# Performance work log

Hardware: AMD Instinct MI355X
Metric: run time of the kernel (lower is better)

## Reference

```python
import jax, jax.numpy as jnp
import numpy as np

B, T, H, HORIZON = 512, 256, 512, 64


def setup_inputs() -> dict:
    key = jax.random.key(0)
    ks = jax.random.split(key, 16)
    s = 1.0 / np.sqrt(H)  # PyTorch LSTM init bound

    def u(k, shape):
        return jax.random.uniform(k, shape, jnp.float32, -s, s)

    return {
        "x": jax.random.normal(ks[0], (B, T, 1), jnp.float32),
        "enc_Wih0": u(ks[1], (4 * H, 1)),
        "enc_Whh0": u(ks[2], (4 * H, H)),
        "enc_b0": u(ks[3], (4 * H,)),
        "enc_Wih1": u(ks[4], (4 * H, H)),
        "enc_Whh1": u(ks[5], (4 * H, H)),
        "enc_b1": u(ks[6], (4 * H,)),
        "dec_Wih0": u(ks[7], (4 * H, 1)),
        "dec_Whh0": u(ks[8], (4 * H, H)),
        "dec_b0": u(ks[9], (4 * H,)),
        "dec_Wih1": u(ks[10], (4 * H, H)),
        "dec_Whh1": u(ks[11], (4 * H, H)),
        "dec_b1": u(ks[12], (4 * H,)),
        "head_W": u(ks[13], (1, H)),
        "head_b": u(ks[14], (1,)),
    }


def _lstm_cell(x_t, h, c, Wih, Whh, b):
    # PyTorch gate order: input, forget, cell(g), output
    gates = x_t @ Wih.T + h @ Whh.T + b  # [B, 4H]
    i, f, g, o = jnp.split(gates, 4, axis=-1)
    i = jax.nn.sigmoid(i)
    f = jax.nn.sigmoid(f)
    g = jnp.tanh(g)
    o = jax.nn.sigmoid(o)
    c_new = f * c + i * g
    return o * jnp.tanh(c_new), c_new


def reference(x, enc_Wih0, enc_Whh0, enc_b0, enc_Wih1, enc_Whh1, enc_b1,
              dec_Wih0, dec_Whh0, dec_b0, dec_Wih1, dec_Whh1, dec_b1,
              head_W, head_b):
    b_sz = x.shape[0]
    hid = enc_Whh0.shape[1]
    z = jnp.zeros((b_sz, hid), x.dtype)

    # ---- encoder: 2-layer LSTM over time, keep only final (h, c) ----
    def enc_step(carry, x_t):
        h0, c0, h1, c1 = carry
        h0, c0 = _lstm_cell(x_t, h0, c0, enc_Wih0, enc_Whh0, enc_b0)
        h1, c1 = _lstm_cell(h0, h1, c1, enc_Wih1, enc_Whh1, enc_b1)
        return (h0, c0, h1, c1), None

    (h0, c0, h1, c1), _ = jax.lax.scan(enc_step, (z, z, z, z),
                                       jnp.swapaxes(x, 0, 1))  # time-major [T,B,1]

    dec_in = x[:, -1, :]  # [B, 1] last observed value

    def dec_step(carry, _):
        h0, c0, h1, c1, inp = carry
        h0, c0 = _lstm_cell(inp, h0, c0, dec_Wih0, dec_Whh0, dec_b0)
        h1, c1 = _lstm_cell(h0, h1, c1, dec_Wih1, dec_Whh1, dec_b1)
        step = h1 @ head_W.T + head_b  # [B, 1]
        return (h0, c0, h1, c1, step), step

    _, steps = jax.lax.scan(dec_step, (h0, c0, h1, c1, dec_in),
                            None, length=HORIZON)  # [HORIZON, B, 1]
    return jnp.swapaxes(steps[..., 0], 0, 1)  # [B, HORIZON]
```

## Files before the change

### kernel.cpp

```cpp
#include <hip/hip_runtime.h>
#include <math.h>

using ushort_t = unsigned short;
using short8 = __attribute__((ext_vector_type(8))) short;
using floatx16 = __attribute__((ext_vector_type(16))) float;
using int4v = __attribute__((ext_vector_type(4))) int;
using int2v = __attribute__((ext_vector_type(2))) int;

constexpr int kB = 512, kT = 256, kH = 512, kHor = 64;
constexpr int NG = 4 * kH;

__device__ __forceinline__ ushort_t f2bf(float v) {
  unsigned u = __builtin_bit_cast(unsigned, v);
  return (ushort_t)((u + 0x7FFFu + ((u >> 16) & 1u)) >> 16);
}
__device__ __forceinline__ float bf2f(ushort_t b) {
  unsigned u = (unsigned)b << 16;
  return __builtin_bit_cast(float, u);
}
__device__ __forceinline__ float sig_(float x) { return 1.0f / (1.0f + __expf(-x)); }

__device__ __forceinline__ void async16(const ushort_t* g, ushort_t* l) {
  __builtin_amdgcn_global_load_lds(
      (const __attribute__((address_space(1))) void*)g,
      (__attribute__((address_space(3))) void*)l, 16, 0, 0);
}

struct UnitP {
  const ushort_t *Whi, *Wlo;
  const ushort_t *B0hi, *B0lo;
  const ushort_t *B1hi, *B1lo;
  const float* bias;
  ushort_t *Hhi, *Hlo;
  int Kw;
};

struct EX {
  const float* xsrc; const float* wx; int xmode; int tcol;
  float* outp; int ocol;
  float* inp_next; const float* headb; int do_init;
  const float* headW; float* head_acc; int do_head;
};

struct Ptrs {
  const float* x;
  const ushort_t *w0eh, *w0el, *w1eh, *w1el;
  const ushort_t *w0dh, *w0dl, *w1dh, *w1dl;
  ushort_t *h0h[2], *h0l[2], *h1h[2], *h1l[2];
  const float *be0, *be1, *bd0, *bd1, *wxe, *wxd;
  float *ib0, *ib1;
  const float *hW, *hb;
  float* out;
  unsigned *bar1, *barR, *barG;
};

__device__ __forceinline__ void run_unit(const UnitP& U, const EX& E, const bool isB,
                                         const int mb, const int nb,
                                         ushort_t* sm, ushort_t* hshi, ushort_t* hslo,
                                         float* creg) {
  const int tid = threadIdx.x;
  const int m0blk = mb * 64;
  const int n0blk = nb * 64;
  const int nkt = U.Kw >> 6;

  const int wv = tid >> 6;
  const int ln = tid & 63;
  const int l31 = ln & 31;
  const int half = ln >> 5;
  const int wm = wv & 1, wn = wv >> 1;
  const int m0w = wm * 32, n0w = wn * 32;

  const int r8 = ln >> 3;
  const int k8s = (ln & 7) ^ r8;
  const bool stA = wv < 2;
  const ushort_t* gsrcA = (wv == 0) ? U.Whi : U.Wlo;
  const ushort_t* b0p = (wv == 2) ? U.B0hi : U.B0lo;
  const ushort_t* b1p = (wv == 2) ? U.B1hi : U.B1lo;
  ushort_t* lwb = &sm[wv * 4096];

  int4v breg[8];

  auto issueW = [&](int kt, int bufsel) {
    ushort_t* lb = lwb + bufsel * 16384;
    const ushort_t* g0 = gsrcA + (size_t)(m0blk + r8) * U.Kw + kt * 64 + k8s * 8;
    #pragma unroll
    for (int i = 0; i < 8; ++i)
      async16(g0 + (size_t)i * 8 * U.Kw, lb + i * 512);
  };
  auto issueB = [&](int kt) {
    const ushort_t* bsrc = (kt < 8) ? b0p : b1p;
    const int col0 = (kt & 7) * 64;
    const ushort_t* g0 = bsrc + (size_t)(n0blk + r8) * kH + col0 + k8s * 8;
    #pragma unroll
    for (int i = 0; i < 8; ++i)
      asm volatile("global_load_dwordx4 %0, %1, off sc0 sc1"
                   : "=v"(breg[i])
                   : "v"(g0 + (size_t)i * 8 * kH)
                   : "memory");
  };
  auto writeB = [&](int bufsel) {
    ushort_t* lb = lwb + bufsel * 16384;
    asm volatile("s_waitcnt vmcnt(0)" ::: "memory");
    #pragma unroll
    for (int i = 0; i < 8; ++i)
      *(int4v*)(lb + i * 512 + ln * 8) = breg[i];
    asm volatile("s_waitcnt lgkmcnt(0)" ::: "memory");
  };

  floatx16 acc;
  #pragma unroll
  for (int i = 0; i < 16; ++i) acc[i] = 0.0f;

  if (stA) issueW(0, 0); else issueB(0);

  for (int kt = 0; kt < nkt; ++kt) {
    const int cur = kt & 1;
    if (kt + 1 < nkt) {
      if (kt > 0) {
        asm volatile("" ::: "memory");
        __builtin_amdgcn_s_barrier();
        asm volatile("" ::: "memory");
      }
      if (stA) {
        issueW(kt + 1, cur ^ 1);
        asm volatile("" ::: "memory");
        __builtin_amdgcn_s_waitcnt(0xF78);
      } else {
        writeB(cur);
        issueB(kt + 1);
      }
    } else {
      if (stA) {
        asm volatile("" ::: "memory");
        __builtin_amdgcn_s_waitcnt(0xF70);
      } else {
        writeB(cur);
      }
    }
    asm volatile("" ::: "memory");
    __builtin_amdgcn_s_barrier();
    asm volatile("" ::: "memory");

    const ushort_t* base = &sm[cur * 16384];
    #pragma unroll
    for (int ks = 0; ks < 4; ++ks) {
      const int k8 = ks * 2 + half;
      const int qa = (m0w + l31) * 8 + (k8 ^ (l31 & 7));
      const int qb = (n0w + l31) * 8 + (k8 ^ (l31 & 7));
      short8 ahi = *(const short8*)(base + qa * 8);
      short8 alo = *(const short8*)(base + 4096 + qa * 8);
      short8 bhi = *(const short8*)(base + 8192 + qb * 8);
      short8 blo = *(const short8*)(base + 12288 + qb * 8);
      acc = __builtin_amdgcn_mfma_f32_32x32x16_bf16(alo, bhi, acc, 0, 0, 0);
      acc = __builtin_amdgcn_mfma_f32_32x32x16_bf16(ahi, blo, acc, 0, 0, 0);
      acc = __builtin_amdgcn_mfma_f32_32x32x16_bf16(ahi, bhi, acc, 0, 0, 0);
    }
  }

  const int jt0 = mb * 16;
  const int ng = n0blk + n0w + l31;
  float xv = 0.0f;
  if (!isB) {
    if (E.xmode == 0) xv = E.xsrc[(size_t)ng * kT + E.tcol];
    else xv = __hip_atomic_load((float*)&E.xsrc[ng], __ATOMIC_RELAXED,
                                __HIP_MEMORY_SCOPE_AGENT);
  }

  #pragma unroll
  for (int rg = 0; rg < 4; ++rg) {
    const int jl = wm * 8 + rg * 2 + half;
    const int jg = jt0 + jl;
    const float4 bi = *(const float4*)&U.bias[jg * 4];
    float gi = acc[rg * 4 + 0] + bi.x;
    float gf = acc[rg * 4 + 1] + bi.y;
    float gg = acc[rg * 4 + 2] + bi.z;
    float go = acc[rg * 4 + 3] + bi.w;
    if (!isB) {
      const float4 wx4 = *(const float4*)&E.wx[jg * 4];
      gi += xv * wx4.x; gf += xv * wx4.y; gg += xv * wx4.z; go += xv * wx4.w;
    }
    const float i_ = sig_(gi), f_ = sig_(gf), g_ = tanhf(gg), o_ = sig_(go);
    const float cn = f_ * creg[rg] + i_ * g_;
    creg[rg] = cn;
    const float hn = o_ * tanhf(cn);
    const ushort_t hhi = f2bf(hn);
    const ushort_t hlo = f2bf(hn - bf2f(hhi));
    const int nbk = n0w + l31;
    hshi[nbk * 18 + jl] = hhi;
    hslo[nbk * 18 + jl] = hlo;
  }
  __syncthreads();

  {
    const int nbk = tid >> 2;
    const int jq = (tid & 3) * 4;
    const unsigned a0 = hshi[nbk * 18 + jq + 0], a1 = hshi[nbk * 18 + jq + 1];
    const unsigned a2 = hshi[nbk * 18 + jq + 2], a3 = hshi[nbk * 18 + jq + 3];
    const unsigned b0 = hslo[nbk * 18 + jq + 0], b1 = hslo[nbk * 18 + jq + 1];
    const unsigned b2 = hslo[nbk * 18 + jq + 2], b3 = hslo[nbk * 18 + jq + 3];
    int2v vh, vl;
    vh[0] = (int)(a0 | (a1 << 16)); vh[1] = (int)(a2 | (a3 << 16));
    vl[0] = (int)(b0 | (b1 << 16)); vl[1] = (int)(b2 | (b3 << 16));
    ushort_t* ph = &U.Hhi[(size_t)(n0blk + nbk) * kH + jt0 + jq];
    ushort_t* pl = &U.Hlo[(size_t)(n0blk + nbk) * kH + jt0 + jq];
    asm volatile("global_store_dwordx2 %0, %1, off sc0 sc1"
                 :: "v"(ph), "v"(vh) : "memory");
    asm volatile("global_store_dwordx2 %0, %1, off sc0 sc1"
                 :: "v"(pl), "v"(vl) : "memory");
  }

  if (isB) {
    if (E.do_head && tid < 64) {
      float s = 0.0f;
      #pragma unroll
      for (int jb = 0; jb < 16; ++jb)
        s += (bf2f(hshi[tid * 18 + jb]) + bf2f(hslo[tid * 18 + jb])) * E.headW[jt0 + jb];
      atomicAdd(&E.head_acc[n0blk + tid], s);
    }
  } else if (mb == 0 && tid < 64) {
    const int n = n0blk + tid;
    if (E.do_init)
      __hip_atomic_store(&E.inp_next[n], E.headb[0], __ATOMIC_RELAXED,
                         __HIP_MEMORY_SCOPE_AGENT);
    if (E.ocol >= 0) {
      const float v = __hip_atomic_load((float*)&E.xsrc[n], __ATOMIC_RELAXED,
                                        __HIP_MEMORY_SCOPE_AGENT);
      E.outp[(size_t)n * kHor + E.ocol] = v;
    }
  }
}

__global__ __launch_bounds__(256, 2) void lstm_persist(Ptrs P) {
  __shared__ __align__(16) ushort_t sm[32768];
  __shared__ ushort_t hshi[64 * 18];
  __shared__ ushort_t hslo[64 * 18];

  const int tid = threadIdx.x;
  const int bx = blockIdx.x;
  const bool isB = bx >= 256;
  const int bid = isB ? bx - 256 : bx;
  const int xs = bid & 7;
  const int q = bid >> 3;
  const int mb = (q >> 3) * 8 + xs;
  const int nb = q & 7;

  float creg[4] = {0.0f, 0.0f, 0.0f, 0.0f};

  int gen = 0;
  auto gbar = [&]() {
    asm volatile("s_waitcnt vmcnt(0)" ::: "memory");
    __syncthreads();
    if (tid == 0) {
      unsigned old = __hip_atomic_fetch_add(&P.bar1[(bx & 63) * 32], 1u,
                         __ATOMIC_RELAXED, __HIP_MEMORY_SCOPE_AGENT);
      if (old == (unsigned)(gen * 8 + 7)) {
        unsigned o2 = __hip_atomic_fetch_add(P.barR, 1u,
                          __ATOMIC_RELAXED, __HIP_MEMORY_SCOPE_AGENT);
        if (o2 == (unsigned)(gen * 64 + 63))
          __hip_atomic_store(P.barG, (unsigned)(gen + 1),
                             __ATOMIC_RELAXED, __HIP_MEMORY_SCOPE_AGENT);
      }
      while (__hip_atomic_load(P.barG, __ATOMIC_RELAXED,
                               __HIP_MEMORY_SCOPE_AGENT) <= (unsigned)gen)
        __builtin_amdgcn_s_sleep(2);
    }
    __syncthreads();
    ++gen;
  };

  for (int p = 0; p <= kT; ++p) {
    const int rd = p & 1, wr = (p + 1) & 1;
    const bool active = isB ? (p >= 1) : (p < kT);
    if (active) {
      UnitP U; EX E = {};
      if (!isB) {
        U = UnitP{P.w0eh, P.w0el, P.h0h[rd], P.h0l[rd], P.h0h[rd], P.h0l[rd],
                  P.be0, P.h0h[wr], P.h0l[wr], 512};
        E.xsrc = P.x; E.wx = P.wxe; E.xmode = 0; E.tcol = p; E.ocol = -1;
      } else {
        U = UnitP{P.w1eh, P.w1el, P.h0h[rd], P.h0l[rd], P.h1h[rd], P.h1l[rd],
                  P.be1, P.h1h[wr], P.h1l[wr], 1024};
        E.ocol = -1;
      }
      run_unit(U, E, isB, mb, nb, sm, hshi, hslo, creg);
    }
    gbar();
  }

  for (int t = 0; t < kHor; ++t) {
    const int r0 = t & 1, w0i = (t + 1) & 1;
    const int r1 = (t + 1) & 1, w1i = t & 1;
    float* ibr = (t & 1) ? P.ib1 : P.ib0;
    float* ibw = (t & 1) ? P.ib0 : P.ib1;
    if (!isB) {
      UnitP U = {P.w0dh, P.w0dl, P.h0h[r0], P.h0l[r0], P.h0h[r0], P.h0l[r0],
                 P.bd0, P.h0h[w0i], P.h0l[w0i], 512};
      EX E = {};
      E.wx = P.wxd;
      if (t == 0) { E.xsrc = P.x; E.xmode = 0; E.tcol = 255; E.ocol = -1; }
      else        { E.xsrc = ibr; E.xmode = 1; E.ocol = t - 1; E.outp = P.out; }
      E.do_init = 1; E.inp_next = ibw; E.headb = P.hb;
      run_unit(U, E, false, mb, nb, sm, hshi, hslo, creg);
    }
    gbar();
    if (isB) {
      UnitP U = {P.w1dh, P.w1dl, P.h0h[w0i], P.h0l[w0i], P.h1h[r1], P.h1l[r1],
                 P.bd1, P.h1h[w1i], P.h1l[w1i], 1024};
      EX E = {};
      E.ocol = -1;
      E.do_head = 1; E.headW = P.hW; E.head_acc = ibw;
      run_unit(U, E, true, mb, nb, sm, hshi, hslo, creg);
    }
    gbar();
  }

  if (!isB && mb == 0 && tid < 64) {
    const int n = nb * 64 + tid;
    P.out[(size_t)n * kHor + 63] =
        __hip_atomic_load(P.ib0 + n, __ATOMIC_RELAXED, __HIP_MEMORY_SCOPE_AGENT);
  }
}

__global__ void prep_w(const float* __restrict__ s0, const float* __restrict__ s1,
                       ushort_t* __restrict__ hi, ushort_t* __restrict__ lo, int Kw) {
  const int k = blockIdx.x * 256 + threadIdx.x;
  const int r = blockIdx.y;
  const int j = r >> 2, g = r & 3;
  const int srow = g * kH + j;
  const float v = (k < kH) ? s0[(size_t)srow * kH + k]
                           : s1[(size_t)srow * kH + (k - kH)];
  const ushort_t h = f2bf(v);
  const ushort_t l = f2bf(v - bf2f(h));
  hi[(size_t)r * Kw + k] = h;
  lo[(size_t)r * Kw + k] = l;
}

__global__ void prep_vec(const float* __restrict__ src, float* __restrict__ dst) {
  const int t = blockIdx.x * 256 + threadIdx.x;
  const int j = t >> 2, g = t & 3;
  dst[t] = src[g * kH + j];
}

__global__ void init_zero(ushort_t* p0, ushort_t* p1, ushort_t* p2, ushort_t* p3,
                          ushort_t* p4, ushort_t* p5, ushort_t* p6, ushort_t* p7) {
  const int i = blockIdx.x * 256 + threadIdx.x;
  p0[i] = 0; p1[i] = 0; p2[i] = 0; p3[i] = 0;
  p4[i] = 0; p5[i] = 0; p6[i] = 0; p7[i] = 0;
}

__global__ void init_bar(unsigned* b) {
  const int i = blockIdx.x * 256 + threadIdx.x;
  if (i < 2112) b[i] = 0;
}

extern "C" void kernel_launch(void* const* d_in, const int* in_sizes, int n_in,
                              void* d_out, int out_size, void* d_ws, size_t ws_size,
                              hipStream_t stream) {
  const float* x     = (const float*)d_in[0];
  const float* eWih0 = (const float*)d_in[1];
  const float* eWhh0 = (const float*)d_in[2];
  const float* eb0   = (const float*)d_in[3];
  const float* eWih1 = (const float*)d_in[4];
  const float* eWhh1 = (const float*)d_in[5];
  const float* eb1   = (const float*)d_in[6];
  const float* dWih0 = (const float*)d_in[7];
  const float* dWhh0 = (const float*)d_in[8];
  const float* db0   = (const float*)d_in[9];
  const float* dWih1 = (const float*)d_in[10];
  const float* dWhh1 = (const float*)d_in[11];
  const float* db1   = (const float*)d_in[12];
  const float* hW    = (const float*)d_in[13];
  const float* hb    = (const float*)d_in[14];
  float* out = (float*)d_out;

  char* w = (char*)d_ws;
  size_t off = 0;
  auto aus = [&](size_t n) { ushort_t* p = (ushort_t*)(w + off); off += ((n * 2 + 255) & ~(size_t)255); return p; };
  auto afl = [&](size_t n) { float* p = (float*)(w + off); off += ((n * 4 + 255) & ~(size_t)255); return p; };

  ushort_t* w0e_hi = aus((size_t)NG * 512); ushort_t* w0e_lo = aus((size_t)NG * 512);
  ushort_t* w1e_hi = aus((size_t)NG * 1024); ushort_t* w1e_lo = aus((size_t)NG * 1024);
  ushort_t* w0d_hi = aus((size_t)NG * 512); ushort_t* w0d_lo = aus((size_t)NG * 512);
  ushort_t* w1d_hi = aus((size_t)NG * 1024); ushort_t* w1d_lo = aus((size_t)NG * 1024);
  ushort_t* h0hi[2] = {aus(kB * kH), aus(kB * kH)};
  ushort_t* h0lo[2] = {aus(kB * kH), aus(kB * kH)};
  ushort_t* h1hi[2] = {aus(kB * kH), aus(kB * kH)};
  ushort_t* h1lo[2] = {aus(kB * kH), aus(kB * kH)};
  float* be0 = afl(NG); float* be1 = afl(NG);
  float* bd0 = afl(NG); float* bd1 = afl(NG);
  float* wxe = afl(NG); float* wxd = afl(NG);
  float* ib0 = afl(kB); float* ib1 = afl(kB);
  unsigned* barb = (unsigned*)(w + off); off += ((2112 * 4 + 255) & ~(size_t)255);

  prep_w<<<dim3(2, NG), 256, 0, stream>>>(eWhh0, eWhh0, w0e_hi, w0e_lo, 512);
  prep_w<<<dim3(4, NG), 256, 0, stream>>>(eWih1, eWhh1, w1e_hi, w1e_lo, 1024);
  prep_w<<<dim3(2, NG), 256, 0, stream>>>(dWhh0, dWhh0, w0d_hi, w0d_lo, 512);
  prep_w<<<dim3(4, NG), 256, 0, stream>>>(dWih1, dWhh1, w1d_hi, w1d_lo, 1024);
  prep_vec<<<8, 256, 0, stream>>>(eb0, be0);
  prep_vec<<<8, 256, 0, stream>>>(eb1, be1);
  prep_vec<<<8, 256, 0, stream>>>(db0, bd0);
  prep_vec<<<8, 256, 0, stream>>>(db1, bd1);
  prep_vec<<<8, 256, 0, stream>>>(eWih0, wxe);
  prep_vec<<<8, 256, 0, stream>>>(dWih0, wxd);
  init_zero<<<1024, 256, 0, stream>>>(h0hi[0], h0hi[1], h0lo[0], h0lo[1],
                                      h1hi[0], h1hi[1], h1lo[0], h1lo[1]);
  init_bar<<<9, 256, 0, stream>>>(barb);

  Ptrs P = {};
  P.x = x;
  P.w0eh = w0e_hi; P.w0el = w0e_lo; P.w1eh = w1e_hi; P.w1el = w1e_lo;
  P.w0dh = w0d_hi; P.w0dl = w0d_lo; P.w1dh = w1d_hi; P.w1dl = w1d_lo;
  P.h0h[0] = h0hi[0]; P.h0h[1] = h0hi[1];
  P.h0l[0] = h0lo[0]; P.h0l[1] = h0lo[1];
  P.h1h[0] = h1hi[0]; P.h1h[1] = h1hi[1];
  P.h1l[0] = h1lo[0]; P.h1l[1] = h1lo[1];
  P.be0 = be0; P.be1 = be1; P.bd0 = bd0; P.bd1 = bd1;
  P.wxe = wxe; P.wxd = wxd;
  P.ib0 = ib0; P.ib1 = ib1;
  P.hW = hW; P.hb = hb;
  P.out = out;
  P.bar1 = barb; P.barR = barb + 2048; P.barG = barb + 2080;

  lstm_persist<<<512, 256, 0, stream>>>(P);
}
```

Baseline: 6.142 ms.

## Double M-tile per block, stream weights from global, triple-buffer hidden state in LDS

Each block now covers 128 gate rows instead of 64, which halves the persistent grid from 512 to 256 blocks and changes the barrier fan-in from 8 to 4 arrivals per slot. Weight fragments are read straight from global memory into registers, so only the hidden-state (B) tiles are staged through LDS, using a three-buffer register-prefetch pipeline. Each wave now runs two 32x32 MFMA accumulators, and the h writeback uses wider 16-byte stores. The aim is fewer blocks to synchronise and less LDS traffic per step. The cost is higher register pressure (launch bounds drop to 1 block per CU) and weight loads that depend on cache hits rather than being coalesced through LDS.

Result: slower. 15.76 ms (+156.6%).

```diff
diff --git a/kernel.cpp b/kernel.cpp
--- a/kernel.cpp
+++ b/kernel.cpp
@@ -5,7 +5,6 @@
 using short8 = __attribute__((ext_vector_type(8))) short;
 using floatx16 = __attribute__((ext_vector_type(16))) float;
 using int4v = __attribute__((ext_vector_type(4))) int;
-using int2v = __attribute__((ext_vector_type(2))) int;
 
 constexpr int kB = 512, kT = 256, kH = 512, kHor = 64;
 constexpr int NG = 4 * kH;
@@ -19,12 +18,6 @@
   return __builtin_bit_cast(float, u);
 }
 __device__ __forceinline__ float sig_(float x) { return 1.0f / (1.0f + __expf(-x)); }
-
-__device__ __forceinline__ void async16(const ushort_t* g, ushort_t* l) {
-  __builtin_amdgcn_global_load_lds(
-      (const __attribute__((address_space(1))) void*)g,
-      (__attribute__((address_space(3))) void*)l, 16, 0, 0);
-}
 
 struct UnitP {
   const ushort_t *Whi, *Wlo;
@@ -59,7 +52,7 @@
                                          ushort_t* sm, ushort_t* hshi, ushort_t* hslo,
                                          float* creg) {
   const int tid = threadIdx.x;
-  const int m0blk = mb * 64;
+  const int m0blk = mb * 128;
   const int n0blk = nb * 64;
   const int nkt = U.Kw >> 6;
 
@@ -68,97 +61,101 @@
   const int l31 = ln & 31;
   const int half = ln >> 5;
   const int wm = wv & 1, wn = wv >> 1;
-  const int m0w = wm * 32, n0w = wn * 32;
-
-  const int r8 = ln >> 3;
-  const int k8s = (ln & 7) ^ r8;
-  const bool stA = wv < 2;
-  const ushort_t* gsrcA = (wv == 0) ? U.Whi : U.Wlo;
-  const ushort_t* b0p = (wv == 2) ? U.B0hi : U.B0lo;
-  const ushort_t* b1p = (wv == 2) ? U.B1hi : U.B1lo;
-  ushort_t* lwb = &sm[wv * 4096];
-
-  int4v breg[8];
-
-  auto issueW = [&](int kt, int bufsel) {
-    ushort_t* lb = lwb + bufsel * 16384;
-    const ushort_t* g0 = gsrcA + (size_t)(m0blk + r8) * U.Kw + kt * 64 + k8s * 8;
-    #pragma unroll
-    for (int i = 0; i < 8; ++i)
-      async16(g0 + (size_t)i * 8 * U.Kw, lb + i * 512);
+
+  const size_t rowA = (size_t)(m0blk + wm * 64 + l31) * U.Kw;
+  const ushort_t* aHi0 = U.Whi + rowA;
+  const ushort_t* aLo0 = U.Wlo + rowA;
+  const ushort_t* aHi1 = aHi0 + (size_t)32 * U.Kw;
+  const ushort_t* aLo1 = aLo0 + (size_t)32 * U.Kw;
+
+  const int sn0 = tid >> 3;
+  const int sk8 = (tid & 7) ^ (sn0 & 7);
+  const size_t g0off = (size_t)(n0blk + sn0) * kH + sk8 * 8;
+  const size_t g1off = g0off + (size_t)32 * kH;
+
+  auto issueB = [&](int ktc, int4v& r0, int4v& r1, int4v& r2, int4v& r3) {
+    const ushort_t* bhiP = (ktc < 8) ? U.B0hi : U.B1hi;
+    const ushort_t* bloP = (ktc < 8) ? U.B0lo : U.B1lo;
+    const int col0 = (ktc & 7) * 64;
+    const ushort_t* p0 = bhiP + g0off + col0;
+    const ushort_t* p1 = bhiP + g1off + col0;
+    const ushort_t* p2 = bloP + g0off + col0;
+    const ushort_t* p3 = bloP + g1off + col0;
+    asm volatile("global_load_dwordx4 %0, %1, off sc0 sc1" : "=v"(r0) : "v"(p0) : "memory");
+    asm volatile("global_load_dwordx4 %0, %1, off sc0 sc1" : "=v"(r1) : "v"(p1) : "memory");
+    asm volatile("global_load_dwordx4 %0, %1, off sc0 sc1" : "=v"(r2) : "v"(p2) : "memory");
+    asm volatile("global_load_dwordx4 %0, %1, off sc0 sc1" : "=v"(r3) : "v"(p3) : "memory");
   };
-  auto issueB = [&](int kt) {
-    const ushort_t* bsrc = (kt < 8) ? b0p : b1p;
-    const int col0 = (kt & 7) * 64;
-    const ushort_t* g0 = bsrc + (size_t)(n0blk + r8) * kH + col0 + k8s * 8;
-    #pragma unroll
-    for (int i = 0; i < 8; ++i)
-      asm volatile("global_load_dwordx4 %0, %1, off sc0 sc1"
-                   : "=v"(breg[i])
-                   : "v"(g0 + (size_t)i * 8 * kH)
-                   : "memory");
+  auto writeBuf = [&](int bufsel, int4v r0, int4v r1, int4v r2, int4v r3) {
+    ushort_t* b = sm + bufsel * 8192;
+    *(int4v*)(b + tid * 8) = r0;
+    *(int4v*)(b + 2048 + tid * 8) = r1;
+    *(int4v*)(b + 4096 + tid * 8) = r2;
+    *(int4v*)(b + 6144 + tid * 8) = r3;
   };
-  auto writeB = [&](int bufsel) {
-    ushort_t* lb = lwb + bufsel * 16384;
-    asm volatile("s_waitcnt vmcnt(0)" ::: "memory");
-    #pragma unroll
-    for (int i = 0; i < 8; ++i)
-      *(int4v*)(lb + i * 512 + ln * 8) = breg[i];
-    asm volatile("s_waitcnt lgkmcnt(0)" ::: "memory");
-  };
-
-  floatx16 acc;
+
+  floatx16 acc0, acc1;
   #pragma unroll
-  for (int i = 0; i < 16; ++i) acc[i] = 0.0f;
-
-  if (stA) issueW(0, 0); else issueB(0);
-
-  for (int kt = 0; kt < nkt; ++kt) {
-    const int cur = kt & 1;
-    if (kt + 1 < nkt) {
-      if (kt > 0) {
-        asm volatile("" ::: "memory");
-        __builtin_amdgcn_s_barrier();
-        asm volatile("" ::: "memory");
-      }
-      if (stA) {
-        issueW(kt + 1, cur ^ 1);
-        asm volatile("" ::: "memory");
-        __builtin_amdgcn_s_waitcnt(0xF78);
-      } else {
-        writeB(cur);
-        issueB(kt + 1);
-      }
-    } else {
-      if (stA) {
-        asm volatile("" ::: "memory");
-        __builtin_amdgcn_s_waitcnt(0xF70);
-      } else {
-        writeB(cur);
-      }
-    }
-    asm volatile("" ::: "memory");
-    __builtin_amdgcn_s_barrier();
-    asm volatile("" ::: "memory");
-
-    const ushort_t* base = &sm[cur * 16384];
+  for (int i = 0; i < 16; ++i) { acc0[i] = 0.0f; acc1[i] = 0.0f; }
+
+  auto compute = [&](int bufsel, int kt) {
+    const ushort_t* base = sm + bufsel * 8192;
     #pragma unroll
     for (int ks = 0; ks < 4; ++ks) {
       const int k8 = ks * 2 + half;
-      const int qa = (m0w + l31) * 8 + (k8 ^ (l31 & 7));
-      const int qb = (n0w + l31) * 8 + (k8 ^ (l31 & 7));
-      short8 ahi = *(const short8*)(base + qa * 8);
-      short8 alo = *(const short8*)(base + 4096 + qa * 8);
-      short8 bhi = *(const short8*)(base + 8192 + qb * 8);
-      short8 blo = *(const short8*)(base + 12288 + qb * 8);
-      acc = __builtin_amdgcn_mfma_f32_32x32x16_bf16(alo, bhi, acc, 0, 0, 0);
-      acc = __builtin_amdgcn_mfma_f32_32x32x16_bf16(ahi, blo, acc, 0, 0, 0);
-      acc = __builtin_amdgcn_mfma_f32_32x32x16_bf16(ahi, bhi, acc, 0, 0, 0);
-    }
-  }
-
-  const int jt0 = mb * 16;
-  const int ng = n0blk + n0w + l31;
+      const int qb = (wn * 32 + l31) * 8 + (k8 ^ (l31 & 7));
+      short8 bhi = *(const short8*)(base + qb * 8);
+      short8 blo = *(const short8*)(base + 4096 + qb * 8);
+      const int off = kt * 64 + k8 * 8;
+      short8 a0h = *(const short8*)(aHi0 + off);
+      short8 a0l = *(const short8*)(aLo0 + off);
+      short8 a1h = *(const short8*)(aHi1 + off);
+      short8 a1l = *(const short8*)(aLo1 + off);
+      acc0 = __builtin_amdgcn_mfma_f32_32x32x16_bf16(a0l, bhi, acc0, 0, 0, 0);
+      acc0 = __builtin_amdgcn_mfma_f32_32x32x16_bf16(a0h, blo, acc0, 0, 0, 0);
+      acc0 = __builtin_amdgcn_mfma_f32_32x32x16_bf16(a0h, bhi, acc0, 0, 0, 0);
+      acc1 = __builtin_amdgcn_mfma_f32_32x32x16_bf16(a1l, bhi, acc1, 0, 0, 0);
+      acc1 = __builtin_amdgcn_mfma_f32_32x32x16_bf16(a1h, blo, acc1, 0, 0, 0);
+      acc1 = __builtin_amdgcn_mfma_f32_32x32x16_bf16(a1h, bhi, acc1, 0, 0, 0);
+    }
+  };
+
+  int4v e0, e1, e2, e3, o0, o1, o2, o3;
+
+  issueB(0, e0, e1, e2, e3);
+  issueB(1, o0, o1, o2, o3);
+  asm volatile("s_waitcnt vmcnt(4)" ::: "memory");
+  writeBuf(0, e0, e1, e2, e3);
+  issueB(2, e0, e1, e2, e3);
+
+  for (int kt = 0; kt < nkt; kt += 2) {
+    {
+      if (kt + 2 < nkt) { asm volatile("s_waitcnt vmcnt(4)" ::: "memory"); }
+      else              { asm volatile("s_waitcnt vmcnt(0)" ::: "memory"); }
+      writeBuf((kt + 1) % 3, o0, o1, o2, o3);
+      asm volatile("s_waitcnt lgkmcnt(0)" ::: "memory");
+      __builtin_amdgcn_s_barrier();
+      asm volatile("" ::: "memory");
+      compute(kt % 3, kt);
+      if (kt + 3 < nkt) issueB(kt + 3, o0, o1, o2, o3);
+    }
+    {
+      const int k2 = kt + 1;
+      if (k2 + 2 < nkt) { asm volatile("s_waitcnt vmcnt(4)" ::: "memory"); }
+      else              { asm volatile("s_waitcnt vmcnt(0)" ::: "memory"); }
+      if (k2 + 1 < nkt) writeBuf((k2 + 1) % 3, e0, e1, e2, e3);
+      asm volatile("s_waitcnt lgkmcnt(0)" ::: "memory");
+      __builtin_amdgcn_s_barrier();
+      asm volatile("" ::: "memory");
+      compute(k2 % 3, k2);
+      if (k2 + 3 < nkt) issueB(k2 + 3, e0, e1, e2, e3);
+    }
+  }
+  asm volatile("s_waitcnt vmcnt(0)" ::: "memory");
+
+  const int jt0 = mb * 32;
+  const int nlane = wn * 32 + l31;
+  const int ng = n0blk + nlane;
   float xv = 0.0f;
   if (!isB) {
     if (E.xmode == 0) xv = E.xsrc[(size_t)ng * kT + E.tcol];
@@ -167,54 +164,50 @@
   }
 
   #pragma unroll
-  for (int rg = 0; rg < 4; ++rg) {
-    const int jl = wm * 8 + rg * 2 + half;
-    const int jg = jt0 + jl;
-    const float4 bi = *(const float4*)&U.bias[jg * 4];
-    float gi = acc[rg * 4 + 0] + bi.x;
-    float gf = acc[rg * 4 + 1] + bi.y;
-    float gg = acc[rg * 4 + 2] + bi.z;
-    float go = acc[rg * 4 + 3] + bi.w;
-    if (!isB) {
-      const float4 wx4 = *(const float4*)&E.wx[jg * 4];
-      gi += xv * wx4.x; gf += xv * wx4.y; gg += xv * wx4.z; go += xv * wx4.w;
-    }
-    const float i_ = sig_(gi), f_ = sig_(gf), g_ = tanhf(gg), o_ = sig_(go);
-    const float cn = f_ * creg[rg] + i_ * g_;
-    creg[rg] = cn;
-    const float hn = o_ * tanhf(cn);
-    const ushort_t hhi = f2bf(hn);
-    const ushort_t hlo = f2bf(hn - bf2f(hhi));
-    const int nbk = n0w + l31;
-    hshi[nbk * 18 + jl] = hhi;
-    hslo[nbk * 18 + jl] = hlo;
+  for (int mt = 0; mt < 2; ++mt) {
+    const floatx16& ac = mt ? acc1 : acc0;
+    #pragma unroll
+    for (int rg = 0; rg < 4; ++rg) {
+      const int jl = wm * 16 + mt * 8 + rg * 2 + half;
+      const int jg = jt0 + jl;
+      const float4 bi = *(const float4*)&U.bias[jg * 4];
+      float gi = ac[rg * 4 + 0] + bi.x;
+      float gf = ac[rg * 4 + 1] + bi.y;
+      float gg = ac[rg * 4 + 2] + bi.z;
+      float go = ac[rg * 4 + 3] + bi.w;
+      if (!isB) {
+        const float4 wx4 = *(const float4*)&E.wx[jg * 4];
+        gi += xv * wx4.x; gf += xv * wx4.y; gg += xv * wx4.z; go += xv * wx4.w;
+      }
+      const float i_ = sig_(gi), f_ = sig_(gf), g_ = tanhf(gg), o_ = sig_(go);
+      const float cn = f_ * creg[mt * 4 + rg] + i_ * g_;
+      creg[mt * 4 + rg] = cn;
+      const float hn = o_ * tanhf(cn);
+      const ushort_t hhi = f2bf(hn);
+      const ushort_t hlo = f2bf(hn - bf2f(hhi));
+      hshi[nlane * 48 + jl] = hhi;
+      hslo[nlane * 48 + jl] = hlo;
+    }
   }
   __syncthreads();
 
   {
-    const int nbk = tid >> 2;
-    const int jq = (tid & 3) * 4;
-    const unsigned a0 = hshi[nbk * 18 + jq + 0], a1 = hshi[nbk * 18 + jq + 1];
-    const unsigned a2 = hshi[nbk * 18 + jq + 2], a3 = hshi[nbk * 18 + jq + 3];
-    const unsigned b0 = hslo[nbk * 18 + jq + 0], b1 = hslo[nbk * 18 + jq + 1];
-    const unsigned b2 = hslo[nbk * 18 + jq + 2], b3 = hslo[nbk * 18 + jq + 3];
-    int2v vh, vl;
-    vh[0] = (int)(a0 | (a1 << 16)); vh[1] = (int)(a2 | (a3 << 16));
-    vl[0] = (int)(b0 | (b1 << 16)); vl[1] = (int)(b2 | (b3 << 16));
-    ushort_t* ph = &U.Hhi[(size_t)(n0blk + nbk) * kH + jt0 + jq];
-    ushort_t* pl = &U.Hlo[(size_t)(n0blk + nbk) * kH + jt0 + jq];
-    asm volatile("global_store_dwordx2 %0, %1, off sc0 sc1"
-                 :: "v"(ph), "v"(vh) : "memory");
-    asm volatile("global_store_dwordx2 %0, %1, off sc0 sc1"
-                 :: "v"(pl), "v"(vl) : "memory");
+    const int nl = tid >> 2;
+    const int jq = (tid & 3) * 8;
+    int4v vh = *(const int4v*)&hshi[nl * 48 + jq];
+    int4v vl = *(const int4v*)&hslo[nl * 48 + jq];
+    ushort_t* ph = &U.Hhi[(size_t)(n0blk + nl) * kH + jt0 + jq];
+    ushort_t* pl = &U.Hlo[(size_t)(n0blk + nl) * kH + jt0 + jq];
+    asm volatile("global_store_dwordx4 %0, %1, off sc0 sc1" :: "v"(ph), "v"(vh) : "memory");
+    asm volatile("global_store_dwordx4 %0, %1, off sc0 sc1" :: "v"(pl), "v"(vl) : "memory");
   }
 
   if (isB) {
     if (E.do_head && tid < 64) {
       float s = 0.0f;
       #pragma unroll
-      for (int jb = 0; jb < 16; ++jb)
-        s += (bf2f(hshi[tid * 18 + jb]) + bf2f(hslo[tid * 18 + jb])) * E.headW[jt0 + jb];
+      for (int jb = 0; jb < 32; ++jb)
+        s += (bf2f(hshi[tid * 48 + jb]) + bf2f(hslo[tid * 48 + jb])) * E.headW[jt0 + jb];
       atomicAdd(&E.head_acc[n0blk + tid], s);
     }
   } else if (mb == 0 && tid < 64) {
@@ -230,21 +223,21 @@
   }
 }
 
-__global__ __launch_bounds__(256, 2) void lstm_persist(Ptrs P) {
-  __shared__ __align__(16) ushort_t sm[32768];
-  __shared__ ushort_t hshi[64 * 18];
-  __shared__ ushort_t hslo[64 * 18];
+__global__ __launch_bounds__(256, 1) void lstm_persist(Ptrs P) {
+  __shared__ __align__(16) ushort_t sm[3 * 8192];
+  __shared__ __align__(16) ushort_t hshi[64 * 48];
+  __shared__ __align__(16) ushort_t hslo[64 * 48];
 
   const int tid = threadIdx.x;
   const int bx = blockIdx.x;
-  const bool isB = bx >= 256;
-  const int bid = isB ? bx - 256 : bx;
+  const bool isB = bx >= 128;
+  const int bid = isB ? bx - 128 : bx;
   const int xs = bid & 7;
   const int q = bid >> 3;
-  const int mb = (q >> 3) * 8 + xs;
+  const int mb = xs + 8 * (q >> 3);
   const int nb = q & 7;
 
-  float creg[4] = {0.0f, 0.0f, 0.0f, 0.0f};
+  float creg[8] = {0.f, 0.f, 0.f, 0.f, 0.f, 0.f, 0.f, 0.f};
 
   int gen = 0;
   auto gbar = [&]() {
@@ -253,7 +246,7 @@
     if (tid == 0) {
       unsigned old = __hip_atomic_fetch_add(&P.bar1[(bx & 63) * 32], 1u,
                          __ATOMIC_RELAXED, __HIP_MEMORY_SCOPE_AGENT);
-      if (old == (unsigned)(gen * 8 + 7)) {
+      if (old == (unsigned)(gen * 4 + 3)) {
         unsigned o2 = __hip_atomic_fetch_add(P.barR, 1u,
                           __ATOMIC_RELAXED, __HIP_MEMORY_SCOPE_AGENT);
         if (o2 == (unsigned)(gen * 64 + 63))
@@ -421,5 +414,5 @@
   P.out = out;
   P.bar1 = barb; P.barR = barb + 2048; P.barG = barb + 2080;
 
-  lstm_persist<<<512, 256, 0, stream>>>(P);
-}
+  lstm_persist<<<256, 256, 0, stream>>>(P);
+}
```

## Spread A/B tile loads across all waves with deeper register prefetch of B

Applied to the files above, without the earlier changes.

Before this, two waves loaded the weight tiles through async LDS loads and the other two waves loaded the hidden-state tiles through registers. Now all four waves share both loads. B tiles are prefetched two k-steps ahead in two register sets, and the loop is unrolled by two with explicit vmcnt waits. The aim is to balance load issue across waves and hide global latency of the coherent hidden-state reads behind MFMA work. In exchange it uses more registers and needs more careful waitcnt bookkeeping, where an error would corrupt results.

Result: slower. 7.050 ms (+14.8%).

```diff
diff --git a/kernel.cpp b/kernel.cpp
--- a/kernel.cpp
+++ b/kernel.cpp
@@ -72,90 +72,111 @@
 
   const int r8 = ln >> 3;
   const int k8s = (ln & 7) ^ r8;
-  const bool stA = wv < 2;
-  const ushort_t* gsrcA = (wv == 0) ? U.Whi : U.Wlo;
-  const ushort_t* b0p = (wv == 2) ? U.B0hi : U.B0lo;
-  const ushort_t* b1p = (wv == 2) ? U.B1hi : U.B1lo;
-  ushort_t* lwb = &sm[wv * 4096];
-
-  int4v breg[8];
-
-  auto issueW = [&](int kt, int bufsel) {
-    ushort_t* lb = lwb + bufsel * 16384;
-    const ushort_t* g0 = gsrcA + (size_t)(m0blk + r8) * U.Kw + kt * 64 + k8s * 8;
+  const ushort_t* gsrcA = (wv < 2) ? U.Whi : U.Wlo;
+  const size_t aRowOff = (size_t)(m0blk + (wv & 1) * 32 + r8) * U.Kw + k8s * 8;
+  const int aLds = ((wv < 2) ? 0 : 4096) + (wv & 1) * 2048;
+
+  auto issueA = [&](int kt, int bufsel) {
+    ushort_t* lb = sm + bufsel * 8192 + aLds;
+    const ushort_t* g0 = gsrcA + aRowOff + kt * 64;
     #pragma unroll
-    for (int i = 0; i < 8; ++i)
+    for (int i = 0; i < 4; ++i)
       async16(g0 + (size_t)i * 8 * U.Kw, lb + i * 512);
   };
-  auto issueB = [&](int kt) {
-    const ushort_t* bsrc = (kt < 8) ? b0p : b1p;
-    const int col0 = (kt & 7) * 64;
-    const ushort_t* g0 = bsrc + (size_t)(n0blk + r8) * kH + col0 + k8s * 8;
-    #pragma unroll
-    for (int i = 0; i < 8; ++i)
-      asm volatile("global_load_dwordx4 %0, %1, off sc0 sc1"
-                   : "=v"(breg[i])
-                   : "v"(g0 + (size_t)i * 8 * kH)
-                   : "memory");
+
+  const int brow = tid >> 3;
+  const int bk8 = (tid & 7) ^ (brow & 7);
+  const size_t bOff0 = (size_t)(n0blk + brow) * kH + bk8 * 8;
+  const size_t bOff1 = bOff0 + (size_t)32 * kH;
+
+  auto issueBset = [&](int ktc, int4v* s) {
+    const ushort_t* bhiP = (ktc < 8) ? U.B0hi : U.B1hi;
+    const ushort_t* bloP = (ktc < 8) ? U.B0lo : U.B1lo;
+    const int col0 = (ktc & 7) * 64;
+    asm volatile("global_load_dwordx4 %0, %1, off sc0 sc1"
+                 : "=v"(s[0]) : "v"(bhiP + bOff0 + col0) : "memory");
+    asm volatile("global_load_dwordx4 %0, %1, off sc0 sc1"
+                 : "=v"(s[1]) : "v"(bhiP + bOff1 + col0) : "memory");
+    asm volatile("global_load_dwordx4 %0, %1, off sc0 sc1"
+                 : "=v"(s[2]) : "v"(bloP + bOff0 + col0) : "memory");
+    asm volatile("global_load_dwordx4 %0, %1, off sc0 sc1"
+                 : "=v"(s[3]) : "v"(bloP + bOff1 + col0) : "memory");
   };
-  auto writeB = [&](int bufsel) {
-    ushort_t* lb = lwb + bufsel * 16384;
-    asm volatile("s_waitcnt vmcnt(0)" ::: "memory");
-    #pragma unroll
-    for (int i = 0; i < 8; ++i)
-      *(int4v*)(lb + i * 512 + ln * 8) = breg[i];
-    asm volatile("s_waitcnt lgkmcnt(0)" ::: "memory");
+  auto writeBset = [&](int bufsel, const int4v* s) {
+    ushort_t* b = sm + 16384 + bufsel * 8192;
+    *(int4v*)(b + tid * 8) = s[0];
+    *(int4v*)(b + 2048 + tid * 8) = s[1];
+    *(int4v*)(b + 4096 + tid * 8) = s[2];
+    *(int4v*)(b + 6144 + tid * 8) = s[3];
   };
 
   floatx16 acc;
   #pragma unroll
   for (int i = 0; i < 16; ++i) acc[i] = 0.0f;
 
-  if (stA) issueW(0, 0); else issueB(0);
-
-  for (int kt = 0; kt < nkt; ++kt) {
-    const int cur = kt & 1;
-    if (kt + 1 < nkt) {
+  auto compute = [&](int bufsel) {
+    const ushort_t* ba = sm + bufsel * 8192;
+    const ushort_t* bb = sm + 16384 + bufsel * 8192;
+    #pragma unroll
+    for (int ks = 0; ks < 4; ++ks) {
+      const int k8 = ks * 2 + half;
+      const int qa = (m0w + l31) * 8 + (k8 ^ (l31 & 7));
+      const int qb = (n0w + l31) * 8 + (k8 ^ (l31 & 7));
+      short8 ahi = *(const short8*)(ba + qa * 8);
+      short8 alo = *(const short8*)(ba + 4096 + qa * 8);
+      short8 bhi = *(const short8*)(bb + qb * 8);
+      short8 blo = *(const short8*)(bb + 4096 + qb * 8);
+      acc = __builtin_amdgcn_mfma_f32_32x32x16_bf16(alo, bhi, acc, 0, 0, 0);
+      acc = __builtin_amdgcn_mfma_f32_32x32x16_bf16(ahi, blo, acc, 0, 0, 0);
+      acc = __builtin_amdgcn_mfma_f32_32x32x16_bf16(ahi, bhi, acc, 0, 0, 0);
+    }
+  };
+
+  int4v s0[4], s1[4];
+
+  issueBset(0, s0);
+  issueBset(1, s1);
+  issueA(0, 0);
+  asm volatile("s_waitcnt vmcnt(8)" ::: "memory");
+  writeBset(0, s0);
+  asm volatile("s_waitcnt lgkmcnt(0)" ::: "memory");
+  issueBset(2, s0);
+
+  for (int kt = 0; kt < nkt; kt += 2) {
+    {
       if (kt > 0) {
         asm volatile("" ::: "memory");
         __builtin_amdgcn_s_barrier();
         asm volatile("" ::: "memory");
       }
-      if (stA) {
-        issueW(kt + 1, cur ^ 1);
-        asm volatile("" ::: "memory");
-        __builtin_amdgcn_s_waitcnt(0xF78);
-      } else {
-        writeB(cur);
-        issueB(kt + 1);
-      }
-    } else {
-      if (stA) {
-        asm volatile("" ::: "memory");
-        __builtin_amdgcn_s_waitcnt(0xF70);
-      } else {
-        writeB(cur);
-      }
-    }
-    asm volatile("" ::: "memory");
-    __builtin_amdgcn_s_barrier();
-    asm volatile("" ::: "memory");
-
-    const ushort_t* base = &sm[cur * 16384];
-    #pragma unroll
-    for (int ks = 0; ks < 4; ++ks) {
-      const int k8 = ks * 2 + half;
-      const int qa = (m0w + l31) * 8 + (k8 ^ (l31 & 7));
-      const int qb = (n0w + l31) * 8 + (k8 ^ (l31 & 7));
-      short8 ahi = *(const short8*)(base + qa * 8);
-      short8 alo = *(const short8*)(base + 4096 + qa * 8);
-      short8 bhi = *(const short8*)(base + 8192 + qb * 8);
-      short8 blo = *(const short8*)(base + 12288 + qb * 8);
-      acc = __builtin_amdgcn_mfma_f32_32x32x16_bf16(alo, bhi, acc, 0, 0, 0);
-      acc = __builtin_amdgcn_mfma_f32_32x32x16_bf16(ahi, blo, acc, 0, 0, 0);
-      acc = __builtin_amdgcn_mfma_f32_32x32x16_bf16(ahi, bhi, acc, 0, 0, 0);
-    }
-  }
+      if (kt + 2 < nkt) { asm volatile("s_waitcnt vmcnt(4)" ::: "memory"); }
+      else              { asm volatile("s_waitcnt vmcnt(0)" ::: "memory"); }
+      writeBset(1, s1);
+      asm volatile("s_waitcnt lgkmcnt(0)" ::: "memory");
+      issueA(kt + 1, 1);
+      if (kt + 3 < nkt) issueBset(kt + 3, s1);
+      asm volatile("" ::: "memory");
+      __builtin_amdgcn_s_barrier();
+      asm volatile("" ::: "memory");
+      compute(0);
+    }
+    {
+      asm volatile("" ::: "memory");
+      __builtin_amdgcn_s_barrier();
+      asm volatile("" ::: "memory");
+      if (kt + 3 < nkt) { asm volatile("s_waitcnt vmcnt(4)" ::: "memory"); }
+      else              { asm volatile("s_waitcnt vmcnt(0)" ::: "memory"); }
+      if (kt + 2 < nkt) writeBset(0, s0);
+      asm volatile("s_waitcnt lgkmcnt(0)" ::: "memory");
+      if (kt + 2 < nkt) issueA(kt + 2, 0);
+      if (kt + 4 < nkt) issueBset(kt + 4, s0);
+      asm volatile("" ::: "memory");
+      __builtin_amdgcn_s_barrier();
+      asm volatile("" ::: "memory");
+      compute(1);
+    }
+  }
+  asm volatile("s_waitcnt vmcnt(0)" ::: "memory");
 
   const int jt0 = mb * 16;
   const int ng = n0blk + n0w + l31;
@@ -232,8 +253,8 @@
 
 __global__ __launch_bounds__(256, 2) void lstm_persist(Ptrs P) {
   __shared__ __align__(16) ushort_t sm[32768];
-  __shared__ ushort_t hshi[64 * 18];
-  __shared__ ushort_t hslo[64 * 18];
+  __shared__ __align__(16) ushort_t hshi[64 * 18];
+  __shared__ __align__(16) ushort_t hslo[64 * 18];
 
   const int tid = threadIdx.x;
   const int bx = blockIdx.x;
```

## Retile LSTM gate GEMM to 128x32 blocks with all waves streaming weights

Applied to the files above, without the earlier changes.

Changes each block's tile from 64 gate rows × 64 batch columns to 128 gate rows × 32 batch columns. The 16×16 grid of blocks per layer becomes 16 row groups by 16 batch groups, and each wave now owns a 32-row slice against the full 32 batch columns. All four waves async-load weight (hi/lo) tiles, and the small hidden-state B tile is loaded cooperatively by all threads through registers. The aim is to spread weight streaming across every wave and shrink the per-block hidden-state traffic. The trade-off is more weight bytes per block per step, a larger LDS footprint (hidden-state staging now aliases the A buffer), and a different wait-count pipeline.

New measurement: 8.746 ms. 42.4% more time.

```diff
diff --git a/kernel.cpp b/kernel.cpp
--- a/kernel.cpp
+++ b/kernel.cpp
@@ -9,6 +9,7 @@
 
 constexpr int kB = 512, kT = 256, kH = 512, kHor = 64;
 constexpr int NG = 4 * kH;
+constexpr int HSP = 48;
 
 __device__ __forceinline__ ushort_t f2bf(float v) {
   unsigned u = __builtin_bit_cast(unsigned, v);
@@ -56,109 +57,103 @@
 
 __device__ __forceinline__ void run_unit(const UnitP& U, const EX& E, const bool isB,
                                          const int mb, const int nb,
-                                         ushort_t* sm, ushort_t* hshi, ushort_t* hslo,
-                                         float* creg) {
+                                         ushort_t* sm, float* creg) {
   const int tid = threadIdx.x;
-  const int m0blk = mb * 64;
-  const int n0blk = nb * 64;
+  const int m0blk = mb * 128;
+  const int n0blk = nb * 32;
   const int nkt = U.Kw >> 6;
 
   const int wv = tid >> 6;
   const int ln = tid & 63;
   const int l31 = ln & 31;
   const int half = ln >> 5;
-  const int wm = wv & 1, wn = wv >> 1;
-  const int m0w = wm * 32, n0w = wn * 32;
+  const int m0w = wv * 32;
 
   const int r8 = ln >> 3;
   const int k8s = (ln & 7) ^ r8;
-  const bool stA = wv < 2;
-  const ushort_t* gsrcA = (wv == 0) ? U.Whi : U.Wlo;
-  const ushort_t* b0p = (wv == 2) ? U.B0hi : U.B0lo;
-  const ushort_t* b1p = (wv == 2) ? U.B1hi : U.B1lo;
-  ushort_t* lwb = &sm[wv * 4096];
-
-  int4v breg[8];
-
-  auto issueW = [&](int kt, int bufsel) {
-    ushort_t* lb = lwb + bufsel * 16384;
-    const ushort_t* g0 = gsrcA + (size_t)(m0blk + r8) * U.Kw + kt * 64 + k8s * 8;
+  const ushort_t* gsrcA = (wv < 2) ? U.Whi : U.Wlo;
+  const size_t aRowOff = (size_t)(m0blk + (wv & 1) * 64 + r8) * U.Kw + k8s * 8;
+  const int aLds = ((wv < 2) ? 0 : 8192) + (wv & 1) * 4096;
+
+  auto issueA = [&](int kt, int bufsel) {
+    ushort_t* lb = sm + bufsel * 16384 + aLds;
+    const ushort_t* g0 = gsrcA + aRowOff + kt * 64;
     #pragma unroll
     for (int i = 0; i < 8; ++i)
       async16(g0 + (size_t)i * 8 * U.Kw, lb + i * 512);
   };
-  auto issueB = [&](int kt) {
-    const ushort_t* bsrc = (kt < 8) ? b0p : b1p;
-    const int col0 = (kt & 7) * 64;
-    const ushort_t* g0 = bsrc + (size_t)(n0blk + r8) * kH + col0 + k8s * 8;
-    #pragma unroll
-    for (int i = 0; i < 8; ++i)
-      asm volatile("global_load_dwordx4 %0, %1, off sc0 sc1"
-                   : "=v"(breg[i])
-                   : "v"(g0 + (size_t)i * 8 * kH)
-                   : "memory");
+
+  const int brow = tid >> 3;
+  const int bk8 = (tid & 7) ^ (brow & 7);
+  const size_t bOff = (size_t)(n0blk + brow) * kH + bk8 * 8;
+
+  int4v rh, rl;
+  auto issueB = [&](int ktc) {
+    const ushort_t* bh = (ktc < 8) ? U.B0hi : U.B1hi;
+    const ushort_t* bl = (ktc < 8) ? U.B0lo : U.B1lo;
+    const int col0 = (ktc & 7) * 64;
+    asm volatile("global_load_dwordx4 %0, %1, off sc0 sc1"
+                 : "=v"(rh) : "v"(bh + bOff + col0) : "memory");
+    asm volatile("global_load_dwordx4 %0, %1, off sc0 sc1"
+                 : "=v"(rl) : "v"(bl + bOff + col0) : "memory");
   };
   auto writeB = [&](int bufsel) {
-    ushort_t* lb = lwb + bufsel * 16384;
-    asm volatile("s_waitcnt vmcnt(0)" ::: "memory");
-    #pragma unroll
-    for (int i = 0; i < 8; ++i)
-      *(int4v*)(lb + i * 512 + ln * 8) = breg[i];
-    asm volatile("s_waitcnt lgkmcnt(0)" ::: "memory");
+    ushort_t* b = sm + 32768 + bufsel * 4096;
+    *(int4v*)(b + tid * 8) = rh;
+    *(int4v*)(b + 2048 + tid * 8) = rl;
   };
 
   floatx16 acc;
   #pragma unroll
   for (int i = 0; i < 16; ++i) acc[i] = 0.0f;
 
-  if (stA) issueW(0, 0); else issueB(0);
-
-  for (int kt = 0; kt < nkt; ++kt) {
-    const int cur = kt & 1;
-    if (kt + 1 < nkt) {
-      if (kt > 0) {
-        asm volatile("" ::: "memory");
-        __builtin_amdgcn_s_barrier();
-        asm volatile("" ::: "memory");
-      }
-      if (stA) {
-        issueW(kt + 1, cur ^ 1);
-        asm volatile("" ::: "memory");
-        __builtin_amdgcn_s_waitcnt(0xF78);
-      } else {
-        writeB(cur);
-        issueB(kt + 1);
-      }
-    } else {
-      if (stA) {
-        asm volatile("" ::: "memory");
-        __builtin_amdgcn_s_waitcnt(0xF70);
-      } else {
-        writeB(cur);
-      }
-    }
-    asm volatile("" ::: "memory");
-    __builtin_amdgcn_s_barrier();
-    asm volatile("" ::: "memory");
-
-    const ushort_t* base = &sm[cur * 16384];
+  auto compute = [&](int bufsel) {
+    const ushort_t* ba = sm + bufsel * 16384;
+    const ushort_t* bb = sm + 32768 + bufsel * 4096;
     #pragma unroll
     for (int ks = 0; ks < 4; ++ks) {
       const int k8 = ks * 2 + half;
       const int qa = (m0w + l31) * 8 + (k8 ^ (l31 & 7));
-      const int qb = (n0w + l31) * 8 + (k8 ^ (l31 & 7));
-      short8 ahi = *(const short8*)(base + qa * 8);
-      short8 alo = *(const short8*)(base + 4096 + qa * 8);
-      short8 bhi = *(const short8*)(base + 8192 + qb * 8);
-      short8 blo = *(const short8*)(base + 12288 + qb * 8);
+      const int qb = l31 * 8 + (k8 ^ (l31 & 7));
+      short8 ahi = *(const short8*)(ba + qa * 8);
+      short8 alo = *(const short8*)(ba + 8192 + qa * 8);
+      short8 bhi = *(const short8*)(bb + qb * 8);
+      short8 blo = *(const short8*)(bb + 2048 + qb * 8);
       acc = __builtin_amdgcn_mfma_f32_32x32x16_bf16(alo, bhi, acc, 0, 0, 0);
       acc = __builtin_amdgcn_mfma_f32_32x32x16_bf16(ahi, blo, acc, 0, 0, 0);
       acc = __builtin_amdgcn_mfma_f32_32x32x16_bf16(ahi, bhi, acc, 0, 0, 0);
     }
-  }
-
-  const int jt0 = mb * 16;
-  const int ng = n0blk + n0w + l31;
+  };
+
+  issueA(0, 0);
+  issueB(0);
+
+  for (int kt = 0; kt < nkt; ++kt) {
+    if (kt > 0) {
+      asm volatile("" ::: "memory");
+      __builtin_amdgcn_s_barrier();
+      asm volatile("" ::: "memory");
+    }
+    if (kt + 1 < nkt) {
+      issueA(kt + 1, (kt + 1) & 1);
+      asm volatile("s_waitcnt vmcnt(8)" ::: "memory");
+    } else {
+      asm volatile("s_waitcnt vmcnt(0)" ::: "memory");
+    }
+    writeB(kt & 1);
+    asm volatile("s_waitcnt lgkmcnt(0)" ::: "memory");
+    if (kt + 1 < nkt) issueB(kt + 1);
+    asm volatile("" ::: "memory");
+    __builtin_amdgcn_s_barrier();
+    asm volatile("" ::: "memory");
+    compute(kt & 1);
+  }
+  asm volatile("s_waitcnt vmcnt(0)" ::: "memory");
+
+  ushort_t* hshi = sm;
+  ushort_t* hslo = sm + 2048;
+  const int jt0 = mb * 32;
+  const int ng = n0blk + l31;
   float xv = 0.0f;
   if (!isB) {
     if (E.xmode == 0) xv = E.xsrc[(size_t)ng * kT + E.tcol];
@@ -168,7 +163,7 @@
 
   #pragma unroll
   for (int rg = 0; rg < 4; ++rg) {
-    const int jl = wm * 8 + rg * 2 + half;
+    const int jl = wv * 8 + rg * 2 + half;
     const int jg = jt0 + jl;
     const float4 bi = *(const float4*)&U.bias[jg * 4];
     float gi = acc[rg * 4 + 0] + bi.x;
@@ -185,24 +180,23 @@
     const float hn = o_ * tanhf(cn);
     const ushort_t hhi = f2bf(hn);
     const ushort_t hlo = f2bf(hn - bf2f(hhi));
-    const int nbk = n0w + l31;
-    hshi[nbk * 18 + jl] = hhi;
-    hslo[nbk * 18 + jl] = hlo;
+    hshi[l31 * HSP + jl] = hhi;
+    hslo[l31 * HSP + jl] = hlo;
   }
   __syncthreads();
 
   {
-    const int nbk = tid >> 2;
-    const int jq = (tid & 3) * 4;
-    const unsigned a0 = hshi[nbk * 18 + jq + 0], a1 = hshi[nbk * 18 + jq + 1];
-    const unsigned a2 = hshi[nbk * 18 + jq + 2], a3 = hshi[nbk * 18 + jq + 3];
-    const unsigned b0 = hslo[nbk * 18 + jq + 0], b1 = hslo[nbk * 18 + jq + 1];
-    const unsigned b2 = hslo[nbk * 18 + jq + 2], b3 = hslo[nbk * 18 + jq + 3];
+    const int nl = tid >> 3;
+    const int jq = (tid & 7) * 4;
+    const unsigned a0 = hshi[nl * HSP + jq + 0], a1 = hshi[nl * HSP + jq + 1];
+    const unsigned a2 = hshi[nl * HSP + jq + 2], a3 = hshi[nl * HSP + jq + 3];
+    const unsigned b0 = hslo[nl * HSP + jq + 0], b1 = hslo[nl * HSP + jq + 1];
+    const unsigned b2 = hslo[nl * HSP + jq + 2], b3 = hslo[nl * HSP + jq + 3];
     int2v vh, vl;
     vh[0] = (int)(a0 | (a1 << 16)); vh[1] = (int)(a2 | (a3 << 16));
     vl[0] = (int)(b0 | (b1 << 16)); vl[1] = (int)(b2 | (b3 << 16));
-    ushort_t* ph = &U.Hhi[(size_t)(n0blk + nbk) * kH + jt0 + jq];
-    ushort_t* pl = &U.Hlo[(size_t)(n0blk + nbk) * kH + jt0 + jq];
+    ushort_t* ph = &U.Hhi[(size_t)(n0blk + nl) * kH + jt0 + jq];
+    ushort_t* pl = &U.Hlo[(size_t)(n0blk + nl) * kH + jt0 + jq];
     asm volatile("global_store_dwordx2 %0, %1, off sc0 sc1"
                  :: "v"(ph), "v"(vh) : "memory");
     asm volatile("global_store_dwordx2 %0, %1, off sc0 sc1"
@@ -210,14 +204,14 @@
   }
 
   if (isB) {
-    if (E.do_head && tid < 64) {
+    if (E.do_head && tid < 32) {
       float s = 0.0f;
       #pragma unroll
-      for (int jb = 0; jb < 16; ++jb)
-        s += (bf2f(hshi[tid * 18 + jb]) + bf2f(hslo[tid * 18 + jb])) * E.headW[jt0 + jb];
+      for (int jb = 0; jb < 32; ++jb)
+        s += (bf2f(hshi[tid * HSP + jb]) + bf2f(hslo[tid * HSP + jb])) * E.headW[jt0 + jb];
       atomicAdd(&E.head_acc[n0blk + tid], s);
     }
-  } else if (mb == 0 && tid < 64) {
+  } else if (mb == 0 && tid < 32) {
     const int n = n0blk + tid;
     if (E.do_init)
       __hip_atomic_store(&E.inp_next[n], E.headb[0], __ATOMIC_RELAXED,
@@ -231,9 +225,7 @@
 }
 
 __global__ __launch_bounds__(256, 2) void lstm_persist(Ptrs P) {
-  __shared__ __align__(16) ushort_t sm[32768];
-  __shared__ ushort_t hshi[64 * 18];
-  __shared__ ushort_t hslo[64 * 18];
+  __shared__ __align__(16) ushort_t sm[40960];
 
   const int tid = threadIdx.x;
   const int bx = blockIdx.x;
@@ -241,8 +233,8 @@
   const int bid = isB ? bx - 256 : bx;
   const int xs = bid & 7;
   const int q = bid >> 3;
-  const int mb = (q >> 3) * 8 + xs;
-  const int nb = q & 7;
+  const int mb = xs + 8 * (q >> 4);
+  const int nb = q & 15;
 
   float creg[4] = {0.0f, 0.0f, 0.0f, 0.0f};
 
@@ -282,7 +274,7 @@
                   P.be1, P.h1h[wr], P.h1l[wr], 1024};
         E.ocol = -1;
       }
-      run_unit(U, E, isB, mb, nb, sm, hshi, hslo, creg);
+      run_unit(U, E, isB, mb, nb, sm, creg);
     }
     gbar();
   }
@@ -300,7 +292,7 @@
       if (t == 0) { E.xsrc = P.x; E.xmode = 0; E.tcol = 255; E.ocol = -1; }
       else        { E.xsrc = ibr; E.xmode = 1; E.ocol = t - 1; E.outp = P.out; }
       E.do_init = 1; E.inp_next = ibw; E.headb = P.hb;
-      run_unit(U, E, false, mb, nb, sm, hshi, hslo, creg);
+      run_unit(U, E, false, mb, nb, sm, creg);
     }
     gbar();
     if (isB) {
@@ -309,13 +301,13 @@
       EX E = {};
       E.ocol = -1;
       E.do_head = 1; E.headW = P.hW; E.head_acc = ibw;
-      run_unit(U, E, true, mb, nb, sm, hshi, hslo, creg);
+      run_unit(U, E, true, mb, nb, sm, creg);
     }
     gbar();
   }
 
-  if (!isB && mb == 0 && tid < 64) {
-    const int n = nb * 64 + tid;
+  if (!isB && mb == 0 && tid < 32) {
+    const int n = nb * 32 + tid;
     P.out[(size_t)n * kHor + 63] =
         __hip_atomic_load(P.ib0 + n, __ATOMIC_RELAXED, __HIP_MEMORY_SCOPE_AGENT);
   }
```
